# Kernel optimization log

Hardware: AMD Instinct MI355X
Metric: run time of the kernel (lower is better)

Reference implementation:

```python
import jax, jax.numpy as jnp
import numpy as np

N = 65536          # particles
E = 524288         # relations (avg degree 8)
RIG = 4096         # rigid instance = particles [0, RIG); fluid = [RIG, N)
PSTEPS = 2
ATTR, STATE, RELD, NF = 3, 6, 1, 128
DT = 1.0 / 60.0
MEAN_P = np.zeros(3, np.float32); STD_P = np.ones(3, np.float32)
MEAN_V = np.zeros(3, np.float32); STD_V = np.ones(3, np.float32)


def _lin(x, w, b):
    return x @ w.T + b  # torch Linear convention: w is [out, in]


def setup_inputs() -> dict:
    key = jax.random.key(0)
    ks = iter(jax.random.split(key, 40))
    d = {}
    d["state"] = jax.random.normal(next(ks), (N, STATE), jnp.float32)
    d["attr"] = jax.random.normal(next(ks), (N, ATTR), jnp.float32)
    d["Ra"] = jax.random.normal(next(ks), (E, RELD), jnp.float32)
    d["rel_recv"] = jax.random.randint(next(ks), (E,), 0, N, jnp.int32)
    d["rel_send"] = jax.random.randint(next(ks), (E,), 0, N, jnp.int32)

    def w(shape):
        return jax.random.normal(next(ks), shape, jnp.float32) / np.sqrt(shape[1])

    d["pe_w0"] = w((NF, ATTR + 2 * STATE)); d["pe_b0"] = jnp.zeros(NF)
    d["pe_w1"] = w((NF, NF)); d["pe_b1"] = jnp.zeros(NF)
    d["re_w0"] = w((NF, 2 * ATTR + 4 * STATE + RELD)); d["re_b0"] = jnp.zeros(NF)
    d["re_w1"] = w((NF, NF)); d["re_b1"] = jnp.zeros(NF)
    d["re_w2"] = w((NF, NF)); d["re_b2"] = jnp.zeros(NF)
    d["rp_w"] = w((NF, 3 * NF)); d["rp_b"] = jnp.zeros(NF)
    d["pp_w"] = w((NF, 2 * NF)); d["pp_b"] = jnp.zeros(NF)
    d["rg_w0"] = w((NF, NF)); d["rg_b0"] = jnp.zeros(NF)
    d["rg_w1"] = w((NF, NF)); d["rg_b1"] = jnp.zeros(NF)
    d["rg_w2"] = w((7, NF)); d["rg_b2"] = jnp.zeros(7)
    d["fl_w0"] = w((NF, NF)); d["fl_b0"] = jnp.zeros(NF)
    d["fl_w1"] = w((NF, NF)); d["fl_b1"] = jnp.zeros(NF)
    d["fl_w2"] = w((3, NF)); d["fl_b2"] = jnp.zeros(3)
    return d


def reference(state, attr, Ra, rel_recv, rel_send,
              pe_w0, pe_b0, pe_w1, pe_b1,
              re_w0, re_b0, re_w1, re_b1, re_w2, re_b2,
              rp_w, rp_b, pp_w, pp_b,
              rg_w0, rg_b0, rg_w1, rg_b1, rg_w2, rg_b2,
              fl_w0, fl_b0, fl_w1, fl_b1, fl_w2, fl_b2):
    relu = jax.nn.relu
    mean_p = jnp.asarray(MEAN_P); std_p = jnp.asarray(STD_P)
    mean_v = jnp.asarray(MEAN_V); std_v = jnp.asarray(STD_V)

    # rigid-body offset (state minus instance centroid for the rigid instance)
    offset = jnp.zeros_like(state).at[:RIG].set(
        state[:RIG] - jnp.mean(state[:RIG], axis=0))
    attr2 = jnp.concatenate([attr, offset], axis=1)        # [N, ATTR+STATE]

    # f_O^enc: particle encoder on [attr2, state]
    pe_in = jnp.concatenate([attr2, state], axis=1)         # [N, 15]
    particle_encode = relu(_lin(relu(_lin(pe_in, pe_w0, pe_b0)), pe_w1, pe_b1))

    # f_R^enc: relation encoder on gathered receiver/sender features
    rel_in = jnp.concatenate([attr2[rel_recv], attr2[rel_send],
                              state[rel_recv], state[rel_send], Ra], axis=1)  # [E, 31]
    h = relu(_lin(rel_in, re_w0, re_b0))
    h = relu(_lin(h, re_w1, re_b1))
    relation_encode = relu(_lin(h, re_w2, re_b2))           # [E, NF]

    # propagation: gather effects -> f_R -> scatter-add -> f_O
    effect = jnp.zeros((N, NF), state.dtype)
    for _ in range(PSTEPS):
        r_eff = effect[rel_recv]                            # [E, NF]
        s_eff = effect[rel_send]                            # [E, NF]
        rel_eff = relu(_lin(jnp.concatenate(
            [relation_encode, r_eff, s_eff], axis=1), rp_w, rp_b))
        agg = jax.ops.segment_sum(rel_eff, rel_recv, num_segments=N)  # Rr @ rel_eff
        effect = relu(_lin(jnp.concatenate(
            [particle_encode, agg], axis=1), pp_w, pp_b))   # residual=False

    # rigid predictor: quaternion + translation of the rigid body
    pooled = jnp.mean(effect[:RIG], axis=0)                 # [NF]
    t = _lin(relu(_lin(relu(_lin(pooled, rg_w0, rg_b0)), rg_w1, rg_b1)), rg_w2, rg_b2)
    q = t[:4] / jnp.linalg.norm(t[:4])
    w, x, y, z = q[0], q[1], q[2], q[3]
    R = jnp.stack([
        jnp.stack([1.0 - 2 * (y * y + z * z), 2 * (x * y + z * w), 2 * (x * z - y * w)]),
        jnp.stack([2 * (x * y - z * w), 1.0 - 2 * (x * x + z * z), 2 * (y * z + x * w)]),
        jnp.stack([2 * (x * z + y * w), 2 * (y * z - x * w), 1.0 - 2 * (x * x + y * y)]),
    ])
    b = t[4:] * std_p
    p0 = state[:RIG, :3] * std_p + mean_p
    c = jnp.mean(p0, axis=0)
    p1 = (p0 - c) @ R + b + c
    v = (p1 - p0) / DT
    pred_rigid = (v - mean_v) / std_v                       # [RIG, 3]

    # fluid predictor: per-particle MLP
    f = relu(_lin(effect[RIG:], fl_w0, fl_b0))
    f = relu(_lin(f, fl_w1, fl_b1))
    pred_fluid = _lin(f, fl_w2, fl_b2)                      # [N-RIG, 3]

    return jnp.concatenate([pred_rigid, pred_fluid], axis=0)  # [N, 3]
```

## Files before the change

kernel.cpp:

```cpp
#include <hip/hip_runtime.h>
#include <hip/hip_bf16.h>
#include <cstdio>

#define N_P   65536
#define N_E   524288
#define RIG_  4096

typedef __attribute__((ext_vector_type(8))) short bf16x8;
typedef __attribute__((ext_vector_type(4))) float f32x4;
typedef unsigned short u16;
typedef unsigned int   u32;

__device__ __forceinline__ u16 f2b(float x) {
    __hip_bfloat16 h = __float2bfloat16(x);
    return *(u16*)&h;
}
__device__ __forceinline__ float b2f(u16 u) {
    union { unsigned u; float f; } c; c.u = ((unsigned)u) << 16; return c.f;
}
__device__ __forceinline__ unsigned pk2(float x, float y) {
    return (unsigned)f2b(x) | ((unsigned)f2b(y) << 16);
}
#define MFMA(a,b,c) __builtin_amdgcn_mfma_f32_16x16x32_bf16((a),(b),(c),0,0,0)

__device__ __forceinline__ void bar_l() {
    asm volatile("s_waitcnt lgkmcnt(0)\n\ts_barrier" ::: "memory");
}

__global__ __launch_bounds__(256) void k_hist(const int* __restrict__ recv,
                                              u32* __restrict__ cnt) {
    int i = blockIdx.x * 256 + threadIdx.x;
    if (i < N_E) atomicAdd(&cnt[recv[i]], 1u);
}
__global__ __launch_bounds__(256) void k_scan1(u32* __restrict__ data,
                                               u32* __restrict__ bsum) {
    __shared__ u32 s[256];
    int t = threadIdx.x, g = blockIdx.x * 256 + t;
    u32 v = data[g];
    s[t] = v; __syncthreads();
    for (int o = 1; o < 256; o <<= 1) {
        u32 x = (t >= o) ? s[t - o] : 0u;
        __syncthreads(); s[t] += x; __syncthreads();
    }
    data[g] = s[t] - v;
    if (t == 255) bsum[blockIdx.x] = s[255];
}
__global__ __launch_bounds__(256) void k_scan2(u32* __restrict__ bsum) {
    __shared__ u32 s[256];
    int t = threadIdx.x;
    u32 v = bsum[t];
    s[t] = v; __syncthreads();
    for (int o = 1; o < 256; o <<= 1) {
        u32 x = (t >= o) ? s[t - o] : 0u;
        __syncthreads(); s[t] += x; __syncthreads();
    }
    bsum[t] = s[t] - v;
}
__global__ __launch_bounds__(256) void k_scan3(u32* __restrict__ data,
                                               const u32* __restrict__ bsum) {
    int g = blockIdx.x * 256 + threadIdx.x;
    data[g] += bsum[blockIdx.x];
}
__global__ __launch_bounds__(256) void k_scatter(const int* __restrict__ recv,
                                                 const int* __restrict__ send,
                                                 u32* __restrict__ head,
                                                 int4* __restrict__ edges) {
    int i = blockIdx.x * 256 + threadIdx.x;
    if (i < N_E) {
        int n = recv[i];
        u32 pos = atomicAdd(&head[n], 1u);
        edges[pos] = make_int4(n, send[i], i, 0);
    }
}

struct CvtJob { const float* src; u16* dst; int n; int mode; int bstart; };
struct CvtArgs { CvtJob j[14]; };

__global__ __launch_bounds__(256) void k_cvt_all(CvtArgs a) {
    int b = blockIdx.x;
    int ji = 0;
    #pragma unroll
    for (int k = 1; k < 14; k++) if (b >= a.j[k].bstart) ji = k;
    CvtJob jb = a.j[ji];
    int i = (b - jb.bstart) * 256 + threadIdx.x;
    if (i >= jb.n) return;
    if (jb.mode == 0) {
        jb.dst[i] = f2b(jb.src[i]);
    } else if (jb.mode == 2) {
        int r = i >> 7;
        jb.dst[i] = (r < 3) ? f2b(jb.src[i]) : 0;
    } else if (jb.mode == 3) {
        int r = i >> 7, c = i & 127;
        jb.dst[i] = f2b(jb.src[r * 384 + c]);
    } else if (jb.mode == 4) {
        int r = i >> 7, c = i & 127;
        jb.dst[i] = f2b(jb.src[r * 256 + c]);
    } else if (jb.mode == 5) {
        int r = i >> 5, c = i & 31;
        float v = 0.f;
        if (c < 9)       v = jb.src[r * 31 + c];
        else if (c < 15) v = jb.src[r * 31 + 18 + (c - 9)];
        jb.dst[i] = f2b(v);
    } else if (jb.mode == 6) {
        int r = i >> 5, c = i & 31;
        float v = 0.f;
        if (c < 9)       v = jb.src[r * 31 + 9 + c];
        else if (c < 15) v = jb.src[r * 31 + 24 + (c - 9)];
        jb.dst[i] = f2b(v);
    } else {
        int r = i >> 5, c = i & 31;
        jb.dst[i] = (c < 15) ? f2b(jb.src[r * 15 + c]) : 0;
    }
}

__global__ __launch_bounds__(256) void k_centroid(const float* __restrict__ state,
                                                  float* __restrict__ cent) {
    int d = blockIdx.x;
    __shared__ float red[256];
    float s = 0.f;
    for (int r = threadIdx.x; r < RIG_; r += 256) s += state[r * 6 + d];
    red[threadIdx.x] = s; __syncthreads();
    for (int o = 128; o > 0; o >>= 1) {
        if (threadIdx.x < o) red[threadIdx.x] += red[threadIdx.x + o];
        __syncthreads();
    }
    if (threadIdx.x == 0) cent[d] = red[0] / (float)RIG_;
}

__global__ __launch_bounds__(256) void k_particle_ext(
        const float* __restrict__ state, const float* __restrict__ attr,
        const float* __restrict__ cent,
        const u16* __restrict__ w0r, const u16* __restrict__ w0s,
        const u16* __restrict__ pew0, const float* __restrict__ pe_b0,
        const u16* __restrict__ pew1, const float* __restrict__ pe_b1,
        const u16* __restrict__ wp,
        u16* __restrict__ P, u16* __restrict__ Q, u16* __restrict__ T) {
    __shared__ float in_s[64][16];
    __shared__ u16 INF[64 * 32];
    __shared__ __align__(16) u16 BUF[64 * 128];
    __shared__ float b0_s[128], b1_s[128];
    int t = threadIdx.x;
    int base = blockIdx.x * 64;
    if (t < 128) { b0_s[t] = pe_b0[t]; b1_s[t] = pe_b1[t]; }
    for (int it = t; it < 64 * 15; it += 256) {
        int r = it / 15, c = it % 15;
        int p = base + r;
        float v;
        if (c < 3)      v = attr[p * 3 + c];
        else if (c < 9) v = (p < RIG_) ? (state[p * 6 + (c - 3)] - cent[c - 3]) : 0.0f;
        else            v = state[p * 6 + (c - 9)];
        in_s[r][c] = v;
    }
    __syncthreads();
    int wv = t >> 6, kq4 = (t >> 4) & 3, m = t & 15;
    {
        int e = wv * 16 + m;
        u16 tmp[8];
        #pragma unroll
        for (int j = 0; j < 8; j++) {
            int k = kq4 * 8 + j;
            tmp[j] = (k < 15) ? f2b(in_s[e][k]) : (u16)0;
        }
        *(uint4*)&INF[((wv * 4 + kq4) * 16 + m) * 8] = *(uint4*)tmp;
    }
    int lane = t & 63, mm = lane & 15, quad = lane >> 4;
    bf16x8 af0 = *(const bf16x8*)&INF[((wv * 4 + quad) * 16 + mm) * 8];
    {
        f32x4 acc[8] = {};
        #pragma unroll
        for (int nt = 0; nt < 8; nt++) {
            bf16x8 bf = *(const bf16x8*)(w0r + (size_t)(nt * 16 + mm) * 32 + quad * 8);
            acc[nt] = MFMA(af0, bf, acc[nt]);
        }
        #pragma unroll
        for (int nt = 0; nt < 8; nt++) {
            int col = nt * 16 + mm;
            #pragma unroll
            for (int rg = 0; rg < 4; rg++) {
                int row = wv * 16 + quad * 4 + rg;
                P[(size_t)(base + row) * 128 + col] = f2b(acc[nt][rg]);
            }
        }
    }
    {
        f32x4 acc[8] = {};
        #pragma unroll
        for (int nt = 0; nt < 8; nt++) {
            bf16x8 bf = *(const bf16x8*)(w0s + (size_t)(nt * 16 + mm) * 32 + quad * 8);
            acc[nt] = MFMA(af0, bf, acc[nt]);
        }
        #pragma unroll
        for (int nt = 0; nt < 8; nt++) {
            int col = nt * 16 + mm;
            #pragma unroll
            for (int rg = 0; rg < 4; rg++) {
                int row = wv * 16 + quad * 4 + rg;
                Q[(size_t)(base + row) * 128 + col] = f2b(acc[nt][rg]);
            }
        }
    }
    {
        f32x4 acc[8] = {};
        #pragma unroll
        for (int nt = 0; nt < 8; nt++) {
            bf16x8 bf = *(const bf16x8*)(pew0 + (size_t)(nt * 16 + mm) * 32 + quad * 8);
            acc[nt] = MFMA(af0, bf, acc[nt]);
        }
        #pragma unroll
        for (int nt = 0; nt < 8; nt++) {
            int col = nt * 16 + mm;
            #pragma unroll
            for (int rg = 0; rg < 4; rg++) {
                BUF[((wv * 16 + (col >> 3)) * 16 + quad * 4 + rg) * 8 + (col & 7)] =
                    f2b(fmaxf(acc[nt][rg] + b0_s[col], 0.f));
            }
        }
    }
    {
        f32x4 acc[8] = {};
        for (int kc = 0; kc < 4; kc++) {
            bf16x8 af = *(const bf16x8*)&BUF[((wv * 16 + kc * 4 + quad) * 16 + mm) * 8];
            #pragma unroll
            for (int nt = 0; nt < 8; nt++) {
                bf16x8 bf = *(const bf16x8*)(pew1 + (size_t)(nt * 16 + mm) * 128 + kc * 32 + quad * 8);
                acc[nt] = MFMA(af, bf, acc[nt]);
            }
        }
        #pragma unroll
        for (int nt = 0; nt < 8; nt++) {
            int col = nt * 16 + mm;
            #pragma unroll
            for (int rg = 0; rg < 4; rg++) {
                BUF[((wv * 16 + (col >> 3)) * 16 + quad * 4 + rg) * 8 + (col & 7)] =
                    f2b(fmaxf(acc[nt][rg] + b1_s[col], 0.f));
            }
        }
    }
    {
        f32x4 acc[8] = {};
        for (int kc = 0; kc < 4; kc++) {
            bf16x8 af = *(const bf16x8*)&BUF[((wv * 16 + kc * 4 + quad) * 16 + mm) * 8];
            #pragma unroll
            for (int nt = 0; nt < 8; nt++) {
                bf16x8 bf = *(const bf16x8*)(wp + (size_t)(nt * 16 + mm) * 128 + kc * 32 + quad * 8);
                acc[nt] = MFMA(af, bf, acc[nt]);
            }
        }
        #pragma unroll
        for (int nt = 0; nt < 8; nt++) {
            int col = nt * 16 + mm;
            #pragma unroll
            for (int rg = 0; rg < 4; rg++) {
                int row = wv * 16 + quad * 4 + rg;
                T[(size_t)(base + row) * 128 + col] = f2b(acc[nt][rg]);
            }
        }
    }
}

__global__ __launch_bounds__(512, 4) void k_rel(
        const u16* __restrict__ P, const u16* __restrict__ Q,
        const float* __restrict__ Ra, const int4* __restrict__ edges,
        const float* __restrict__ re_w0_raw, const float* __restrict__ b0,
        const u16* __restrict__ w1b, const float* __restrict__ b1,
        const u16* __restrict__ w2b, const float* __restrict__ b2,
        const u16* __restrict__ wreb, const float* __restrict__ rpb,
        u16* __restrict__ Z, float* __restrict__ agg) {
    __shared__ __align__(16) u16 BUFA[64 * 136];
    __shared__ __align__(16) u16 BUFB[64 * 136];
    __shared__ int rv_s[2][64];
    __shared__ float wRa_s[128], b0_s[128], rpb_s[128];
    int t = threadIdx.x;
    if (t < 128) {
        wRa_s[t] = re_w0_raw[t * 31 + 30];
        b0_s[t] = b0[t]; rpb_s[t] = rpb[t];
    }
    int w = t >> 6, lane = t & 63, mm = lane & 15, quad = lane >> 4;
    int colw = w * 16 + mm;
    bf16x8 W1f[4], W2f[4], WEf[4];
    #pragma unroll
    for (int kc = 0; kc < 4; kc++) {
        W1f[kc] = *(const bf16x8*)(w1b  + (size_t)colw * 128 + kc * 32 + quad * 8);
        W2f[kc] = *(const bf16x8*)(w2b  + (size_t)colw * 128 + kc * 32 + quad * 8);
        WEf[kc] = *(const bf16x8*)(wreb + (size_t)colw * 128 + kc * 32 + quad * 8);
    }
    float b1c = b1[colw], b2c = b2[colw];
    int es = t >> 3, cs2 = (t & 7) * 2;
    int egs = es >> 4, ms = es & 15;
    int sseg = t >> 7, cseg = t & 127;
    int zrow = t >> 3, zc0 = (t & 7) * 16;
    const long NT = N_E / 64;
    const long stride = gridDim.x;

    long tile = blockIdx.x;
    uint4 upC0, upC1, uqC0, uqC1; float raC; int rvC;
    {
        long nb = tile * 64;
        int4 e = edges[nb + es];
        rvC = edges[nb + (t & 63)].x;
        raC = Ra[e.z];
        upC0 = *(const uint4*)(P + (size_t)e.x * 128 + (size_t)cs2 * 8);
        upC1 = *(const uint4*)(P + (size_t)e.x * 128 + (size_t)(cs2 + 1) * 8);
        uqC0 = *(const uint4*)(Q + (size_t)e.y * 128 + (size_t)cs2 * 8);
        uqC1 = *(const uint4*)(Q + (size_t)e.y * 128 + (size_t)(cs2 + 1) * 8);
    }
    __syncthreads();
    int p = 0;
    for (; tile < NT; tile += stride) {
        long base = tile * 64;
        long ntile = tile + stride;
        bool hn = ntile < NT;
        int4 eN = make_int4(0, 0, 0, 0); int rvN = 0;
        if (hn) {
            long nb = ntile * 64;
            eN  = edges[nb + es];
            rvN = edges[nb + (t & 63)].x;
        }
        if (t < 64) rv_s[p][t] = rvC;
        {
            #pragma unroll
            for (int ci = 0; ci < 2; ci++) {
                int kq = cs2 + ci;
                uint4 up = ci ? upC1 : upC0;
                uint4 uq = ci ? uqC1 : uqC0;
                const u16* pp = (const u16*)&up; const u16* qq = (const u16*)&uq;
                u16 outv[8];
                #pragma unroll
                for (int j = 0; j < 8; j++) {
                    int c = kq * 8 + j;
                    float v = b2f(pp[j]) + b2f(qq[j]) + raC * wRa_s[c] + b0_s[c];
                    outv[j] = f2b(fmaxf(v, 0.f));
                }
                *(uint4*)&BUFA[((egs * 16 + kq) * 16 + ms) * 8] = *(uint4*)outv;
            }
        }
        bar_l();
        uint4 upN0{}, upN1{}, uqN0{}, uqN1{}; float raN = 0.f;
        if (hn) {
            raN  = Ra[eN.z];
            upN0 = *(const uint4*)(P + (size_t)eN.x * 128 + (size_t)cs2 * 8);
            upN1 = *(const uint4*)(P + (size_t)eN.x * 128 + (size_t)(cs2 + 1) * 8);
            uqN0 = *(const uint4*)(Q + (size_t)eN.y * 128 + (size_t)cs2 * 8);
            uqN1 = *(const uint4*)(Q + (size_t)eN.y * 128 + (size_t)(cs2 + 1) * 8);
        }
        {
            f32x4 acc[4] = {};
            #pragma unroll
            for (int eg = 0; eg < 4; eg++)
                #pragma unroll
                for (int kc = 0; kc < 4; kc++) {
                    bf16x8 af = *(const bf16x8*)&BUFA[((eg * 16 + kc * 4 + quad) * 16 + mm) * 8];
                    acc[eg] = MFMA(af, W1f[kc], acc[eg]);
                }
            #pragma unroll
            for (int eg = 0; eg < 4; eg++)
                #pragma unroll
                for (int rg = 0; rg < 4; rg++)
                    BUFB[((eg * 16 + (colw >> 3)) * 16 + quad * 4 + rg) * 8 + (colw & 7)] =
                        f2b(fmaxf(acc[eg][rg] + b1c, 0.f));
        }
        bar_l();
        {
            f32x4 acc[4] = {};
            #pragma unroll
            for (int eg = 0; eg < 4; eg++)
                #pragma unroll
                for (int kc = 0; kc < 4; kc++) {
                    bf16x8 af = *(const bf16x8*)&BUFB[((eg * 16 + kc * 4 + quad) * 16 + mm) * 8];
                    acc[eg] = MFMA(af, W2f[kc], acc[eg]);
                }
            #pragma unroll
            for (int eg = 0; eg < 4; eg++)
                #pragma unroll
                for (int rg = 0; rg < 4; rg++)
                    BUFA[((eg * 16 + (colw >> 3)) * 16 + quad * 4 + rg) * 8 + (colw & 7)] =
                        f2b(fmaxf(acc[eg][rg] + b2c, 0.f));
        }
        bar_l();
        {
            f32x4 zacc[4] = {};
            #pragma unroll
            for (int eg = 0; eg < 4; eg++)
                #pragma unroll
                for (int kc = 0; kc < 4; kc++) {
                    bf16x8 af = *(const bf16x8*)&BUFA[((eg * 16 + kc * 4 + quad) * 16 + mm) * 8];
                    zacc[eg] = MFMA(af, WEf[kc], zacc[eg]);
                }
            #pragma unroll
            for (int eg = 0; eg < 4; eg++)
                #pragma unroll
                for (int rg = 0; rg < 4; rg++)
                    BUFB[(eg * 16 + quad * 4 + rg) * 136 + colw] = f2b(zacc[eg][rg]);
        }
        bar_l();
        {
            uint4 z0 = *(const uint4*)&BUFB[zrow * 136 + zc0];
            uint4 z1 = *(const uint4*)&BUFB[zrow * 136 + zc0 + 8];
            *(uint4*)&Z[(base + zrow) * 128 + zc0]     = z0;
            *(uint4*)&Z[(base + zrow) * 128 + zc0 + 8] = z1;
        }
        {
            int r0 = sseg * 16;
            int cur = rv_s[p][r0];
            float a = fmaxf(b2f(BUFB[r0 * 136 + cseg]) + rpb_s[cseg], 0.f);
            bool first = true;
            for (int rr = r0 + 1; rr < r0 + 16; rr++) {
                int n = rv_s[p][rr];
                float v = fmaxf(b2f(BUFB[rr * 136 + cseg]) + rpb_s[cseg], 0.f);
                if (n == cur) a += v;
                else {
                    if (first) atomicAdd(&agg[(size_t)cur * 128 + cseg], a);
                    else       agg[(size_t)cur * 128 + cseg] = a;
                    first = false; cur = n; a = v;
                }
            }
            atomicAdd(&agg[(size_t)cur * 128 + cseg], a);
        }
        if (hn) { upC0 = upN0; upC1 = upN1; uqC0 = uqN0; uqC1 = uqN1; raC = raN; rvC = rvN; }
        p ^= 1;
    }
}

__global__ __launch_bounds__(512, 4) void k_node2(
        const float* __restrict__ agg, const u16* __restrict__ T,
        const u16* __restrict__ wab, const float* __restrict__ ppb,
        const u16* __restrict__ wrb, const u16* __restrict__ wsb,
        u16* __restrict__ U, u16* __restrict__ V) {
    __shared__ __align__(16) u16 BUFA[64 * 128];
    __shared__ __align__(16) u16 BUFB[64 * 128];
    int t = threadIdx.x;
    int w = t >> 6, lane = t & 63, mm = lane & 15, quad = lane >> 4;
    int colw = w * 16 + mm;
    bf16x8 WAf[4], WRf[4], WSf[4];
    #pragma unroll
    for (int kc = 0; kc < 4; kc++) {
        WAf[kc] = *(const bf16x8*)(wab + (size_t)colw * 128 + kc * 32 + quad * 8);
        WRf[kc] = *(const bf16x8*)(wrb + (size_t)colw * 128 + kc * 32 + quad * 8);
        WSf[kc] = *(const bf16x8*)(wsb + (size_t)colw * 128 + kc * 32 + quad * 8);
    }
    float ppbc = ppb[colw];
    int es = t >> 3, cs2 = (t & 7) * 2;
    int egs = es >> 4, ms = es & 15;
    const int NTL = N_P / 64;
    for (int tile = blockIdx.x; tile < NTL; tile += gridDim.x) {
        long base = (long)tile * 64;
        __syncthreads();
        #pragma unroll
        for (int ci = 0; ci < 2; ci++) {
            int kq = cs2 + ci;
            const float* src = agg + (base + es) * 128 + kq * 8;
            float4 f0 = *(const float4*)src, f1 = *(const float4*)(src + 4);
            uint4 v;
            v.x = pk2(f0.x, f0.y); v.y = pk2(f0.z, f0.w);
            v.z = pk2(f1.x, f1.y); v.w = pk2(f1.z, f1.w);
            *(uint4*)&BUFA[((egs * 16 + kq) * 16 + ms) * 8] = v;
        }
        bar_l();
        {
            f32x4 acc[4] = {};
            #pragma unroll
            for (int eg = 0; eg < 4; eg++)
                #pragma unroll
                for (int kc = 0; kc < 4; kc++) {
                    bf16x8 af = *(const bf16x8*)&BUFA[((eg * 16 + kc * 4 + quad) * 16 + mm) * 8];
                    acc[eg] = MFMA(af, WAf[kc], acc[eg]);
                }
            #pragma unroll
            for (int eg = 0; eg < 4; eg++)
                #pragma unroll
                for (int rg = 0; rg < 4; rg++) {
                    long row = base + eg * 16 + quad * 4 + rg;
                    float v = acc[eg][rg] + b2f(T[row * 128 + colw]) + ppbc;
                    BUFB[((eg * 16 + (colw >> 3)) * 16 + quad * 4 + rg) * 8 + (colw & 7)] =
                        f2b(fmaxf(v, 0.f));
                }
        }
        bar_l();
        {
            f32x4 au[4] = {}, av[4] = {};
            #pragma unroll
            for (int eg = 0; eg < 4; eg++)
                #pragma unroll
                for (int kc = 0; kc < 4; kc++) {
                    bf16x8 af = *(const bf16x8*)&BUFB[((eg * 16 + kc * 4 + quad) * 16 + mm) * 8];
                    au[eg] = MFMA(af, WRf[kc], au[eg]);
                    av[eg] = MFMA(af, WSf[kc], av[eg]);
                }
            #pragma unroll
            for (int eg = 0; eg < 4; eg++)
                #pragma unroll
                for (int rg = 0; rg < 4; rg++) {
                    long row = base + eg * 16 + quad * 4 + rg;
                    U[row * 128 + colw] = f2b(au[eg][rg]);
                    V[row * 128 + colw] = f2b(av[eg][rg]);
                }
        }
    }
}

#define HPAD 136
__global__ __launch_bounds__(256) void k_node2fl(
        const float* __restrict__ agg, const u16* __restrict__ T,
        const u16* __restrict__ wab, const float* __restrict__ ppb,
        float* __restrict__ pooledsum,
        const u16* __restrict__ w0b, const float* __restrict__ b0,
        const u16* __restrict__ w1b, const float* __restrict__ b1,
        const u16* __restrict__ w2b, const float* __restrict__ b2,
        float* __restrict__ out) {
    __shared__ __align__(16) u16 H[64 * HPAD];
    int t = threadIdx.x;
    long base = (long)blockIdx.x * 64;
    bool fluid = (base >= RIG_);
    int wv = t >> 6, kq4 = (t >> 4) & 3, m = t & 15;
    {
        long node = base + wv * 16 + m;
        #pragma unroll
        for (int i = 0; i < 4; i++) {
            int kq = kq4 + 4 * i;
            const float* src = agg + node * 128 + kq * 8;
            float4 f0 = *(const float4*)src, f1 = *(const float4*)(src + 4);
            uint4 v;
            v.x = pk2(f0.x, f0.y); v.y = pk2(f0.z, f0.w);
            v.z = pk2(f1.x, f1.y); v.w = pk2(f1.z, f1.w);
            *(uint4*)&H[((wv * 16 + kq) * 16 + m) * 8] = v;
        }
    }
    int lane = t & 63, mm = lane & 15, quad = lane >> 4;
    f32x4 acc[8] = {};
    for (int kc = 0; kc < 4; kc++) {
        bf16x8 af = *(const bf16x8*)&H[((wv * 16 + kc * 4 + quad) * 16 + mm) * 8];
        #pragma unroll
        for (int nt = 0; nt < 8; nt++) {
            bf16x8 bf = *(const bf16x8*)(wab + (size_t)(nt * 16 + mm) * 128 + kc * 32 + quad * 8);
            acc[nt] = MFMA(af, bf, acc[nt]);
        }
    }
    __syncthreads();
    #pragma unroll
    for (int nt = 0; nt < 8; nt++) {
        int col = nt * 16 + mm;
        #pragma unroll
        for (int rg = 0; rg < 4; rg++) {
            long row = base + wv * 16 + quad * 4 + rg;
            float v = acc[nt][rg] + b2f(T[row * 128 + col]) + ppb[col];
            H[(wv * 16 + quad * 4 + rg) * HPAD + col] = f2b(fmaxf(v, 0.f));
        }
    }
    if (!fluid) {
        bar_l();
        int col = t & 127, half = t >> 7;
        float s = 0.f;
        for (int r = half * 32; r < half * 32 + 32; r++)
            s += b2f(H[r * HPAD + col]);
        atomicAdd(&pooledsum[col], s);
        return;
    }
    {
        f32x4 a8[8] = {};
        for (int kc = 0; kc < 4; kc++) {
            bf16x8 af = *(const bf16x8*)&H[(wv * 16 + mm) * HPAD + kc * 32 + quad * 8];
            #pragma unroll
            for (int nt = 0; nt < 8; nt++) {
                bf16x8 bf = *(const bf16x8*)(w0b + (size_t)(nt * 16 + mm) * 128 + kc * 32 + quad * 8);
                a8[nt] = MFMA(af, bf, a8[nt]);
            }
        }
        #pragma unroll
        for (int nt = 0; nt < 8; nt++) {
            int col = nt * 16 + mm;
            float bv = b0[col];
            #pragma unroll
            for (int rg = 0; rg < 4; rg++) {
                int row = wv * 16 + quad * 4 + rg;
                H[row * HPAD + col] = f2b(fmaxf(a8[nt][rg] + bv, 0.f));
            }
        }
    }
    {
        f32x4 a8[8] = {};
        for (int kc = 0; kc < 4; kc++) {
            bf16x8 af = *(const bf16x8*)&H[(wv * 16 + mm) * HPAD + kc * 32 + quad * 8];
            #pragma unroll
            for (int nt = 0; nt < 8; nt++) {
                bf16x8 bf = *(const bf16x8*)(w1b + (size_t)(nt * 16 + mm) * 128 + kc * 32 + quad * 8);
                a8[nt] = MFMA(af, bf, a8[nt]);
            }
        }
        #pragma unroll
        for (int nt = 0; nt < 8; nt++) {
            int col = nt * 16 + mm;
            float bv = b1[col];
            #pragma unroll
            for (int rg = 0; rg < 4; rg++) {
                int row = wv * 16 + quad * 4 + rg;
                H[row * HPAD + col] = f2b(fmaxf(a8[nt][rg] + bv, 0.f));
            }
        }
    }
    {
        f32x4 a1 = {};
        for (int kc = 0; kc < 4; kc++) {
            bf16x8 af = *(const bf16x8*)&H[(wv * 16 + mm) * HPAD + kc * 32 + quad * 8];
            bf16x8 bf = *(const bf16x8*)(w2b + (size_t)mm * 128 + kc * 32 + quad * 8);
            a1 = MFMA(af, bf, a1);
        }
        if (mm < 3) {
            float bv = b2[mm];
            #pragma unroll
            for (int rg = 0; rg < 4; rg++) {
                long row = base + wv * 16 + quad * 4 + rg;
                out[row * 3 + mm] = a1[rg] + bv;
            }
        }
    }
}

__global__ __launch_bounds__(256) void k_edge2(
        const u16* __restrict__ Z, const u16* __restrict__ U, const u16* __restrict__ V,
        const int4* __restrict__ edges,
        const float* __restrict__ rpb, float* __restrict__ agg) {
    __shared__ __align__(16) u16 S16[64 * 136];
    __shared__ int rv_s[64];
    __shared__ float rpb_s[128];
    int t = threadIdx.x;
    long base = (long)blockIdx.x * 64;
    if (t < 64) rv_s[t] = edges[base + t].x;
    if (t < 128) rpb_s[t] = rpb[t];
    int r = t >> 2, q = t & 3;
    int4 er = edges[base + r];
    long zb = (base + r) * 128;
    size_t ub = (size_t)er.x * 128, vb = (size_t)er.y * 128;
    bar_l();
    #pragma unroll
    for (int i = 0; i < 4; i++) {
        int c0 = q * 32 + i * 8;
        uint4 uz = *(const uint4*)(Z + zb + c0);
        uint4 uu = *(const uint4*)(U + ub + c0);
        uint4 uv = *(const uint4*)(V + vb + c0);
        const u16* zz = (const u16*)&uz; const u16* pu = (const u16*)&uu; const u16* pv = (const u16*)&uv;
        u16 o[8];
        #pragma unroll
        for (int j = 0; j < 8; j++)
            o[j] = f2b(fmaxf(b2f(zz[j]) + b2f(pu[j]) + b2f(pv[j]) + rpb_s[c0 + j], 0.f));
        *(uint4*)&S16[r * 136 + c0] = *(uint4*)o;
    }
    bar_l();
    {
        int s = t >> 7, col = t & 127;
        int r0 = s * 32;
        int cur = rv_s[r0];
        float a = b2f(S16[r0 * 136 + col]);
        bool first = true;
        for (int rr = r0 + 1; rr < r0 + 32; rr++) {
            int n = rv_s[rr];
            float v = b2f(S16[rr * 136 + col]);
            if (n == cur) a += v;
            else {
                if (first) atomicAdd(&agg[(size_t)cur * 128 + col], a);
                else       agg[(size_t)cur * 128 + col] = a;
                first = false; cur = n; a = v;
            }
        }
        atomicAdd(&agg[(size_t)cur * 128 + col], a);
    }
}

__global__ __launch_bounds__(128) void k_rigid_head(
        const float* __restrict__ pooledsum,
        const float* __restrict__ w0, const float* __restrict__ b0,
        const float* __restrict__ w1, const float* __restrict__ b1,
        const float* __restrict__ w2, const float* __restrict__ b2,
        float* __restrict__ rig) {
    __shared__ float pl[128], ha[128], hb[128], tv[7];
    int t = threadIdx.x;
    pl[t] = pooledsum[t] * (1.0f / (float)RIG_);
    __syncthreads();
    float a = b0[t];
    for (int k = 0; k < 128; k++) a += w0[t * 128 + k] * pl[k];
    ha[t] = fmaxf(a, 0.f);
    __syncthreads();
    a = b1[t];
    for (int k = 0; k < 128; k++) a += w1[t * 128 + k] * ha[k];
    hb[t] = fmaxf(a, 0.f);
    __syncthreads();
    if (t < 7) {
        float s = b2[t];
        for (int k = 0; k < 128; k++) s += w2[t * 128 + k] * hb[k];
        tv[t] = s;
    }
    __syncthreads();
    if (t == 0) {
        float w = tv[0], x = tv[1], y = tv[2], z = tv[3];
        float n = sqrtf(w * w + x * x + y * y + z * z);
        w /= n; x /= n; y /= n; z /= n;
        rig[0] = 1.f - 2.f * (y * y + z * z); rig[1] = 2.f * (x * y + z * w); rig[2] = 2.f * (x * z - y * w);
        rig[3] = 2.f * (x * y - z * w); rig[4] = 1.f - 2.f * (x * x + z * z); rig[5] = 2.f * (y * z + x * w);
        rig[6] = 2.f * (x * z + y * w); rig[7] = 2.f * (y * z - x * w); rig[8] = 1.f - 2.f * (x * x + y * y);
        rig[9] = tv[4]; rig[10] = tv[5]; rig[11] = tv[6];
    }
}

__global__ __launch_bounds__(256) void k_rigid_out(
        const float* __restrict__ state, const float* __restrict__ cent,
        const float* __restrict__ rig, float* __restrict__ out) {
    int i = blockIdx.x * 256 + threadIdx.x;
    if (i >= RIG_) return;
    float p0[3], d[3];
    #pragma unroll
    for (int k = 0; k < 3; k++) { p0[k] = state[i * 6 + k]; d[k] = p0[k] - cent[k]; }
    #pragma unroll
    for (int j = 0; j < 3; j++) {
        float p1 = rig[0 * 3 + j] * d[0] + rig[1 * 3 + j] * d[1] + rig[2 * 3 + j] * d[2]
                 + rig[9 + j] + cent[j];
        out[i * 3 + j] = (p1 - p0[j]) * 60.0f;
    }
}

extern "C" void kernel_launch(void* const* d_in, const int* in_sizes, int n_in,
                              void* d_out, int out_size, void* d_ws, size_t ws_size,
                              hipStream_t stream) {
    const float* state = (const float*)d_in[0];
    const float* attr  = (const float*)d_in[1];
    const float* Ra    = (const float*)d_in[2];
    const int*   recv  = (const int*)d_in[3];
    const int*   send  = (const int*)d_in[4];
    const float* pe_w0 = (const float*)d_in[5];  const float* pe_b0 = (const float*)d_in[6];
    const float* pe_w1 = (const float*)d_in[7];  const float* pe_b1 = (const float*)d_in[8];
    const float* re_w0 = (const float*)d_in[9];  const float* re_b0 = (const float*)d_in[10];
    const float* re_w1 = (const float*)d_in[11]; const float* re_b1 = (const float*)d_in[12];
    const float* re_w2 = (const float*)d_in[13]; const float* re_b2 = (const float*)d_in[14];
    const float* rp_w  = (const float*)d_in[15]; const float* rp_b  = (const float*)d_in[16];
    const float* pp_w  = (const float*)d_in[17]; const float* pp_b  = (const float*)d_in[18];
    const float* rg_w0 = (const float*)d_in[19]; const float* rg_b0 = (const float*)d_in[20];
    const float* rg_w1 = (const float*)d_in[21]; const float* rg_b1 = (const float*)d_in[22];
    const float* rg_w2 = (const float*)d_in[23]; const float* rg_b2 = (const float*)d_in[24];
    const float* fl_w0 = (const float*)d_in[25]; const float* fl_b0 = (const float*)d_in[26];
    const float* fl_w1 = (const float*)d_in[27]; const float* fl_b1 = (const float*)d_in[28];
    const float* fl_w2 = (const float*)d_in[29]; const float* fl_b2 = (const float*)d_in[30];
    float* out = (float*)d_out;

    char* p = (char*)d_ws;
    auto alloc = [&](size_t bytes) { char* r = p; p += (bytes + 255) / 256 * 256; return r; };
    float* cent    = (float*)alloc(8 * 4);
    float* pooled  = (float*)alloc(128 * 4);
    float* rig     = (float*)alloc(16 * 4);
    u32*   rowhead = (u32*)alloc((size_t)N_P * 4);
    u32*   bsum    = (u32*)alloc(256 * 4);
    int4*  edges   = (int4*)alloc((size_t)N_E * 16);
    float* agg     = (float*)alloc((size_t)N_P * 128 * 4);
    u16*   Z       = (u16*)alloc((size_t)N_E * 128 * 2);
    u16*   T       = (u16*)alloc((size_t)N_P * 128 * 2);
    u16*   P       = (u16*)alloc((size_t)N_P * 128 * 2);
    u16*   Q       = (u16*)alloc((size_t)N_P * 128 * 2);
    u16*   wreb    = (u16*)alloc(128 * 128 * 2);
    u16*   wrb     = (u16*)alloc(128 * 128 * 2);
    u16*   wsb     = (u16*)alloc(128 * 128 * 2);
    u16*   wpb     = (u16*)alloc(128 * 128 * 2);
    u16*   wab     = (u16*)alloc(128 * 128 * 2);
    u16*   rw1b    = (u16*)alloc(128 * 128 * 2);
    u16*   rw2b    = (u16*)alloc(128 * 128 * 2);
    u16*   pew1b   = (u16*)alloc(128 * 128 * 2);
    u16*   flw0b   = (u16*)alloc(128 * 128 * 2);
    u16*   flw1b   = (u16*)alloc(128 * 128 * 2);
    u16*   flw2b   = (u16*)alloc(16 * 128 * 2);
    u16*   w0rb    = (u16*)alloc(128 * 32 * 2);
    u16*   w0sb    = (u16*)alloc(128 * 32 * 2);
    u16*   pew0b   = (u16*)alloc(128 * 32 * 2);
    size_t need = (size_t)(p - (char*)d_ws);
    if (ws_size < need) {
        fprintf(stderr, "kernel_launch: ws_size %zu < needed %zu\n", ws_size, need);
        return;
    }
    u16* U = P; u16* V = Q;

    hipMemsetAsync(rowhead, 0, (size_t)N_P * 4, stream);
    k_hist<<<N_E / 256, 256, 0, stream>>>(recv, rowhead);
    k_scan1<<<N_P / 256, 256, 0, stream>>>(rowhead, bsum);
    k_scan2<<<1, 256, 0, stream>>>(bsum);
    k_scan3<<<N_P / 256, 256, 0, stream>>>(rowhead, bsum);
    k_scatter<<<N_E / 256, 256, 0, stream>>>(recv, send, rowhead, edges);

    CvtArgs ca;
    int bs = 0;
    auto addjob = [&](int idx, const float* s, u16* d, int n, int mode) {
        ca.j[idx] = {s, d, n, mode, bs};
        bs += (n + 255) / 256;
    };
    addjob(0,  rp_w,        wreb,  128 * 128, 3);
    addjob(1,  rp_w + 128,  wrb,   128 * 128, 3);
    addjob(2,  rp_w + 256,  wsb,   128 * 128, 3);
    addjob(3,  pp_w,        wpb,   128 * 128, 4);
    addjob(4,  pp_w + 128,  wab,   128 * 128, 4);
    addjob(5,  re_w1,       rw1b,  128 * 128, 0);
    addjob(6,  re_w2,       rw2b,  128 * 128, 0);
    addjob(7,  pe_w1,       pew1b, 128 * 128, 0);
    addjob(8,  fl_w0,       flw0b, 128 * 128, 0);
    addjob(9,  fl_w1,       flw1b, 128 * 128, 0);
    addjob(10, fl_w2,       flw2b, 16 * 128,  2);
    addjob(11, re_w0,       w0rb,  128 * 32,  5);
    addjob(12, re_w0,       w0sb,  128 * 32,  6);
    addjob(13, pe_w0,       pew0b, 128 * 32,  7);
    k_cvt_all<<<bs, 256, 0, stream>>>(ca);

    k_centroid<<<6, 256, 0, stream>>>(state, cent);
    k_particle_ext<<<N_P / 64, 256, 0, stream>>>(state, attr, cent,
                                                 w0rb, w0sb, pew0b, pe_b0,
                                                 pew1b, pe_b1, wpb, P, Q, T);

    hipMemsetAsync(agg, 0, (size_t)N_P * 128 * 4, stream);
    k_rel<<<512, 512, 0, stream>>>(P, Q, Ra, edges,
                                   re_w0, re_b0, rw1b, re_b1, rw2b, re_b2,
                                   wreb, rp_b, Z, agg);
    k_node2<<<512, 512, 0, stream>>>(agg, T, wab, pp_b, wrb, wsb, U, V);

    hipMemsetAsync(agg, 0, (size_t)N_P * 128 * 4, stream);
    hipMemsetAsync(pooled, 0, 128 * 4, stream);
    k_edge2<<<N_E / 64, 256, 0, stream>>>(Z, U, V, edges, rp_b, agg);
    k_node2fl<<<N_P / 64, 256, 0, stream>>>(agg, T, wab, pp_b, pooled,
                                            flw0b, fl_b0, flw1b, fl_b1,
                                            flw2b, fl_b2, out);

    k_rigid_head<<<1, 128, 0, stream>>>(pooled, rg_w0, rg_b0, rg_w1, rg_b1, rg_w2, rg_b2, rig);
    k_rigid_out<<<(RIG_ + 255) / 256, 256, 0, stream>>>(state, cent, rig, out);
}
```

Before: 513.0 us.

## Make particle encoder and fluid head persistent with register-resident weight fragments

Converts k_particle_ext and k_node2fl into persistent 512-thread kernels over a 512-block grid. Each wave owns a 16-column output slice and keeps its weight fragments in registers across tiles, instead of re-reading the full weight matrices from global memory for every 64-row tile. Each wave now computes all four 16-row groups of a tile for its column slice, using double LDS buffers and block barriers between layers. The rigid pooling reduction is redone with wave shuffles. This raises register pressure and adds extra barriers per tile.

```diff
diff --git a/kernel.cpp b/kernel.cpp
--- a/kernel.cpp
+++ b/kernel.cpp
@@ -127,7 +127,7 @@
     if (threadIdx.x == 0) cent[d] = red[0] / (float)RIG_;
 }
 
-__global__ __launch_bounds__(256) void k_particle_ext(
+__global__ __launch_bounds__(512, 4) void k_particle_ext(
         const float* __restrict__ state, const float* __restrict__ attr,
         const float* __restrict__ cent,
         const u16* __restrict__ w0r, const u16* __restrict__ w0s,
@@ -137,123 +137,114 @@
         u16* __restrict__ P, u16* __restrict__ Q, u16* __restrict__ T) {
     __shared__ float in_s[64][16];
     __shared__ u16 INF[64 * 32];
-    __shared__ __align__(16) u16 BUF[64 * 128];
-    __shared__ float b0_s[128], b1_s[128];
+    __shared__ __align__(16) u16 BUFA[64 * 128];
+    __shared__ __align__(16) u16 BUFB[64 * 128];
     int t = threadIdx.x;
-    int base = blockIdx.x * 64;
-    if (t < 128) { b0_s[t] = pe_b0[t]; b1_s[t] = pe_b1[t]; }
-    for (int it = t; it < 64 * 15; it += 256) {
-        int r = it / 15, c = it % 15;
-        int p = base + r;
-        float v;
-        if (c < 3)      v = attr[p * 3 + c];
-        else if (c < 9) v = (p < RIG_) ? (state[p * 6 + (c - 3)] - cent[c - 3]) : 0.0f;
-        else            v = state[p * 6 + (c - 9)];
-        in_s[r][c] = v;
-    }
-    __syncthreads();
-    int wv = t >> 6, kq4 = (t >> 4) & 3, m = t & 15;
-    {
-        int e = wv * 16 + m;
-        u16 tmp[8];
+    int w = t >> 6, lane = t & 63, mm = lane & 15, quad = lane >> 4;
+    int colw = w * 16 + mm;
+    bf16x8 W0Rf = *(const bf16x8*)(w0r  + (size_t)colw * 32 + quad * 8);
+    bf16x8 W0Sf = *(const bf16x8*)(w0s  + (size_t)colw * 32 + quad * 8);
+    bf16x8 PE0f = *(const bf16x8*)(pew0 + (size_t)colw * 32 + quad * 8);
+    bf16x8 PE1f[4], WPf[4];
+    #pragma unroll
+    for (int kc = 0; kc < 4; kc++) {
+        PE1f[kc] = *(const bf16x8*)(pew1 + (size_t)colw * 128 + kc * 32 + quad * 8);
+        WPf[kc]  = *(const bf16x8*)(wp   + (size_t)colw * 128 + kc * 32 + quad * 8);
+    }
+    float b0c = pe_b0[colw], b1c = pe_b1[colw];
+    const int NTL = N_P / 64;
+    for (int tile = blockIdx.x; tile < NTL; tile += gridDim.x) {
+        int base = tile * 64;
+        bar_l();
+        for (int it = t; it < 64 * 15; it += 512) {
+            int r = it / 15, c = it % 15;
+            int p = base + r;
+            float v;
+            if (c < 3)      v = attr[p * 3 + c];
+            else if (c < 9) v = (p < RIG_) ? (state[p * 6 + (c - 3)] - cent[c - 3]) : 0.0f;
+            else            v = state[p * 6 + (c - 9)];
+            in_s[r][c] = v;
+        }
+        bar_l();
+        if (t < 256) {
+            int wv = t >> 6, kq4 = (t >> 4) & 3, m = t & 15;
+            int e = wv * 16 + m;
+            u16 tmp[8];
+            #pragma unroll
+            for (int j = 0; j < 8; j++) {
+                int k = kq4 * 8 + j;
+                tmp[j] = (k < 15) ? f2b(in_s[e][k]) : (u16)0;
+            }
+            *(uint4*)&INF[((wv * 4 + kq4) * 16 + m) * 8] = *(uint4*)tmp;
+        }
+        bar_l();
+        bf16x8 af0[4];
         #pragma unroll
-        for (int j = 0; j < 8; j++) {
-            int k = kq4 * 8 + j;
-            tmp[j] = (k < 15) ? f2b(in_s[e][k]) : (u16)0;
-        }
-        *(uint4*)&INF[((wv * 4 + kq4) * 16 + m) * 8] = *(uint4*)tmp;
-    }
-    int lane = t & 63, mm = lane & 15, quad = lane >> 4;
-    bf16x8 af0 = *(const bf16x8*)&INF[((wv * 4 + quad) * 16 + mm) * 8];
-    {
-        f32x4 acc[8] = {};
-        #pragma unroll
-        for (int nt = 0; nt < 8; nt++) {
-            bf16x8 bf = *(const bf16x8*)(w0r + (size_t)(nt * 16 + mm) * 32 + quad * 8);
-            acc[nt] = MFMA(af0, bf, acc[nt]);
-        }
-        #pragma unroll
-        for (int nt = 0; nt < 8; nt++) {
-            int col = nt * 16 + mm;
-            #pragma unroll
-            for (int rg = 0; rg < 4; rg++) {
-                int row = wv * 16 + quad * 4 + rg;
-                P[(size_t)(base + row) * 128 + col] = f2b(acc[nt][rg]);
-            }
-        }
-    }
-    {
-        f32x4 acc[8] = {};
-        #pragma unroll
-        for (int nt = 0; nt < 8; nt++) {
-            bf16x8 bf = *(const bf16x8*)(w0s + (size_t)(nt * 16 + mm) * 32 + quad * 8);
-            acc[nt] = MFMA(af0, bf, acc[nt]);
-        }
-        #pragma unroll
-        for (int nt = 0; nt < 8; nt++) {
-            int col = nt * 16 + mm;
-            #pragma unroll
-            for (int rg = 0; rg < 4; rg++) {
-                int row = wv * 16 + quad * 4 + rg;
-                Q[(size_t)(base + row) * 128 + col] = f2b(acc[nt][rg]);
-            }
-        }
-    }
-    {
-        f32x4 acc[8] = {};
-        #pragma unroll
-        for (int nt = 0; nt < 8; nt++) {
-            bf16x8 bf = *(const bf16x8*)(pew0 + (size_t)(nt * 16 + mm) * 32 + quad * 8);
-            acc[nt] = MFMA(af0, bf, acc[nt]);
-        }
-        #pragma unroll
-        for (int nt = 0; nt < 8; nt++) {
-            int col = nt * 16 + mm;
-            #pragma unroll
-            for (int rg = 0; rg < 4; rg++) {
-                BUF[((wv * 16 + (col >> 3)) * 16 + quad * 4 + rg) * 8 + (col & 7)] =
-                    f2b(fmaxf(acc[nt][rg] + b0_s[col], 0.f));
-            }
-        }
-    }
-    {
-        f32x4 acc[8] = {};
-        for (int kc = 0; kc < 4; kc++) {
-            bf16x8 af = *(const bf16x8*)&BUF[((wv * 16 + kc * 4 + quad) * 16 + mm) * 8];
-            #pragma unroll
-            for (int nt = 0; nt < 8; nt++) {
-                bf16x8 bf = *(const bf16x8*)(pew1 + (size_t)(nt * 16 + mm) * 128 + kc * 32 + quad * 8);
-                acc[nt] = MFMA(af, bf, acc[nt]);
-            }
-        }
-        #pragma unroll
-        for (int nt = 0; nt < 8; nt++) {
-            int col = nt * 16 + mm;
-            #pragma unroll
-            for (int rg = 0; rg < 4; rg++) {
-                BUF[((wv * 16 + (col >> 3)) * 16 + quad * 4 + rg) * 8 + (col & 7)] =
-                    f2b(fmaxf(acc[nt][rg] + b1_s[col], 0.f));
-            }
-        }
-    }
-    {
-        f32x4 acc[8] = {};
-        for (int kc = 0; kc < 4; kc++) {
-            bf16x8 af = *(const bf16x8*)&BUF[((wv * 16 + kc * 4 + quad) * 16 + mm) * 8];
-            #pragma unroll
-            for (int nt = 0; nt < 8; nt++) {
-                bf16x8 bf = *(const bf16x8*)(wp + (size_t)(nt * 16 + mm) * 128 + kc * 32 + quad * 8);
-                acc[nt] = MFMA(af, bf, acc[nt]);
-            }
-        }
-        #pragma unroll
-        for (int nt = 0; nt < 8; nt++) {
-            int col = nt * 16 + mm;
-            #pragma unroll
-            for (int rg = 0; rg < 4; rg++) {
-                int row = wv * 16 + quad * 4 + rg;
-                T[(size_t)(base + row) * 128 + col] = f2b(acc[nt][rg]);
-            }
+        for (int eg = 0; eg < 4; eg++)
+            af0[eg] = *(const bf16x8*)&INF[((eg * 4 + quad) * 16 + mm) * 8];
+        {
+            f32x4 a[4] = {};
+            #pragma unroll
+            for (int eg = 0; eg < 4; eg++) a[eg] = MFMA(af0[eg], W0Rf, a[eg]);
+            #pragma unroll
+            for (int eg = 0; eg < 4; eg++)
+                #pragma unroll
+                for (int rg = 0; rg < 4; rg++)
+                    P[(size_t)(base + eg * 16 + quad * 4 + rg) * 128 + colw] = f2b(a[eg][rg]);
+        }
+        {
+            f32x4 a[4] = {};
+            #pragma unroll
+            for (int eg = 0; eg < 4; eg++) a[eg] = MFMA(af0[eg], W0Sf, a[eg]);
+            #pragma unroll
+            for (int eg = 0; eg < 4; eg++)
+                #pragma unroll
+                for (int rg = 0; rg < 4; rg++)
+                    Q[(size_t)(base + eg * 16 + quad * 4 + rg) * 128 + colw] = f2b(a[eg][rg]);
+        }
+        {
+            f32x4 a[4] = {};
+            #pragma unroll
+            for (int eg = 0; eg < 4; eg++) a[eg] = MFMA(af0[eg], PE0f, a[eg]);
+            #pragma unroll
+            for (int eg = 0; eg < 4; eg++)
+                #pragma unroll
+                for (int rg = 0; rg < 4; rg++)
+                    BUFA[((eg * 16 + (colw >> 3)) * 16 + quad * 4 + rg) * 8 + (colw & 7)] =
+                        f2b(fmaxf(a[eg][rg] + b0c, 0.f));
+        }
+        bar_l();
+        {
+            f32x4 a[4] = {};
+            #pragma unroll
+            for (int eg = 0; eg < 4; eg++)
+                #pragma unroll
+                for (int kc = 0; kc < 4; kc++) {
+                    bf16x8 af = *(const bf16x8*)&BUFA[((eg * 16 + kc * 4 + quad) * 16 + mm) * 8];
+                    a[eg] = MFMA(af, PE1f[kc], a[eg]);
+                }
+            #pragma unroll
+            for (int eg = 0; eg < 4; eg++)
+                #pragma unroll
+                for (int rg = 0; rg < 4; rg++)
+                    BUFB[((eg * 16 + (colw >> 3)) * 16 + quad * 4 + rg) * 8 + (colw & 7)] =
+                        f2b(fmaxf(a[eg][rg] + b1c, 0.f));
+        }
+        bar_l();
+        {
+            f32x4 a[4] = {};
+            #pragma unroll
+            for (int eg = 0; eg < 4; eg++)
+                #pragma unroll
+                for (int kc = 0; kc < 4; kc++) {
+                    bf16x8 af = *(const bf16x8*)&BUFB[((eg * 16 + kc * 4 + quad) * 16 + mm) * 8];
+                    a[eg] = MFMA(af, WPf[kc], a[eg]);
+                }
+            #pragma unroll
+            for (int eg = 0; eg < 4; eg++)
+                #pragma unroll
+                for (int rg = 0; rg < 4; rg++)
+                    T[(size_t)(base + eg * 16 + quad * 4 + rg) * 128 + colw] = f2b(a[eg][rg]);
         }
     }
 }
@@ -498,8 +489,7 @@
     }
 }
 
-#define HPAD 136
-__global__ __launch_bounds__(256) void k_node2fl(
+__global__ __launch_bounds__(512, 4) void k_node2fl(
         const float* __restrict__ agg, const u16* __restrict__ T,
         const u16* __restrict__ wab, const float* __restrict__ ppb,
         float* __restrict__ pooledsum,
@@ -507,109 +497,119 @@
         const u16* __restrict__ w1b, const float* __restrict__ b1,
         const u16* __restrict__ w2b, const float* __restrict__ b2,
         float* __restrict__ out) {
-    __shared__ __align__(16) u16 H[64 * HPAD];
+    __shared__ __align__(16) u16 BUFA[64 * 128];
+    __shared__ __align__(16) u16 BUFB[64 * 128];
     int t = threadIdx.x;
-    long base = (long)blockIdx.x * 64;
-    bool fluid = (base >= RIG_);
-    int wv = t >> 6, kq4 = (t >> 4) & 3, m = t & 15;
-    {
-        long node = base + wv * 16 + m;
+    int w = t >> 6, lane = t & 63, mm = lane & 15, quad = lane >> 4;
+    int colw = w * 16 + mm;
+    bf16x8 WAf[4], W0f[4], W1f[4];
+    #pragma unroll
+    for (int kc = 0; kc < 4; kc++) {
+        WAf[kc] = *(const bf16x8*)(wab + (size_t)colw * 128 + kc * 32 + quad * 8);
+        W0f[kc] = *(const bf16x8*)(w0b + (size_t)colw * 128 + kc * 32 + quad * 8);
+        W1f[kc] = *(const bf16x8*)(w1b + (size_t)colw * 128 + kc * 32 + quad * 8);
+    }
+    float ppbc = ppb[colw], b0c = b0[colw], b1c = b1[colw];
+    int es = t >> 3, cs2 = (t & 7) * 2;
+    int egs = es >> 4, ms = es & 15;
+    const int NTL = N_P / 64;
+    for (int tile = blockIdx.x; tile < NTL; tile += gridDim.x) {
+        long base = (long)tile * 64;
+        bool fluid = base >= RIG_;
+        bar_l();
         #pragma unroll
-        for (int i = 0; i < 4; i++) {
-            int kq = kq4 + 4 * i;
-            const float* src = agg + node * 128 + kq * 8;
+        for (int ci = 0; ci < 2; ci++) {
+            int kq = cs2 + ci;
+            const float* src = agg + (base + es) * 128 + kq * 8;
             float4 f0 = *(const float4*)src, f1 = *(const float4*)(src + 4);
             uint4 v;
             v.x = pk2(f0.x, f0.y); v.y = pk2(f0.z, f0.w);
             v.z = pk2(f1.x, f1.y); v.w = pk2(f1.z, f1.w);
-            *(uint4*)&H[((wv * 16 + kq) * 16 + m) * 8] = v;
-        }
-    }
-    int lane = t & 63, mm = lane & 15, quad = lane >> 4;
-    f32x4 acc[8] = {};
-    for (int kc = 0; kc < 4; kc++) {
-        bf16x8 af = *(const bf16x8*)&H[((wv * 16 + kc * 4 + quad) * 16 + mm) * 8];
+            *(uint4*)&BUFA[((egs * 16 + kq) * 16 + ms) * 8] = v;
+        }
+        bar_l();
+        f32x4 acc[4] = {};
         #pragma unroll
-        for (int nt = 0; nt < 8; nt++) {
-            bf16x8 bf = *(const bf16x8*)(wab + (size_t)(nt * 16 + mm) * 128 + kc * 32 + quad * 8);
-            acc[nt] = MFMA(af, bf, acc[nt]);
-        }
-    }
-    __syncthreads();
-    #pragma unroll
-    for (int nt = 0; nt < 8; nt++) {
-        int col = nt * 16 + mm;
+        for (int eg = 0; eg < 4; eg++)
+            #pragma unroll
+            for (int kc = 0; kc < 4; kc++) {
+                bf16x8 af = *(const bf16x8*)&BUFA[((eg * 16 + kc * 4 + quad) * 16 + mm) * 8];
+                acc[eg] = MFMA(af, WAf[kc], acc[eg]);
+            }
+        if (!fluid) {
+            float s = 0.f;
+            #pragma unroll
+            for (int eg = 0; eg < 4; eg++)
+                #pragma unroll
+                for (int rg = 0; rg < 4; rg++) {
+                    long row = base + eg * 16 + quad * 4 + rg;
+                    float v = acc[eg][rg] + b2f(T[row * 128 + colw]) + ppbc;
+                    s += b2f(f2b(fmaxf(v, 0.f)));
+                }
+            s += __shfl_xor(s, 16);
+            s += __shfl_xor(s, 32);
+            if (quad == 0) atomicAdd(&pooledsum[colw], s);
+            continue;
+        }
         #pragma unroll
-        for (int rg = 0; rg < 4; rg++) {
-            long row = base + wv * 16 + quad * 4 + rg;
-            float v = acc[nt][rg] + b2f(T[row * 128 + col]) + ppb[col];
-            H[(wv * 16 + quad * 4 + rg) * HPAD + col] = f2b(fmaxf(v, 0.f));
-        }
-    }
-    if (!fluid) {
-        bar_l();
-        int col = t & 127, half = t >> 7;
-        float s = 0.f;
-        for (int r = half * 32; r < half * 32 + 32; r++)
-            s += b2f(H[r * HPAD + col]);
-        atomicAdd(&pooledsum[col], s);
-        return;
-    }
-    {
-        f32x4 a8[8] = {};
-        for (int kc = 0; kc < 4; kc++) {
-            bf16x8 af = *(const bf16x8*)&H[(wv * 16 + mm) * HPAD + kc * 32 + quad * 8];
-            #pragma unroll
-            for (int nt = 0; nt < 8; nt++) {
-                bf16x8 bf = *(const bf16x8*)(w0b + (size_t)(nt * 16 + mm) * 128 + kc * 32 + quad * 8);
-                a8[nt] = MFMA(af, bf, a8[nt]);
+        for (int eg = 0; eg < 4; eg++)
+            #pragma unroll
+            for (int rg = 0; rg < 4; rg++) {
+                long row = base + eg * 16 + quad * 4 + rg;
+                float v = acc[eg][rg] + b2f(T[row * 128 + colw]) + ppbc;
+                BUFB[((eg * 16 + (colw >> 3)) * 16 + quad * 4 + rg) * 8 + (colw & 7)] =
+                    f2b(fmaxf(v, 0.f));
             }
-        }
-        #pragma unroll
-        for (int nt = 0; nt < 8; nt++) {
-            int col = nt * 16 + mm;
-            float bv = b0[col];
-            #pragma unroll
-            for (int rg = 0; rg < 4; rg++) {
-                int row = wv * 16 + quad * 4 + rg;
-                H[row * HPAD + col] = f2b(fmaxf(a8[nt][rg] + bv, 0.f));
+        bar_l();
+        {
+            f32x4 a[4] = {};
+            #pragma unroll
+            for (int eg = 0; eg < 4; eg++)
+                #pragma unroll
+                for (int kc = 0; kc < 4; kc++) {
+                    bf16x8 af = *(const bf16x8*)&BUFB[((eg * 16 + kc * 4 + quad) * 16 + mm) * 8];
+                    a[eg] = MFMA(af, W0f[kc], a[eg]);
+                }
+            #pragma unroll
+            for (int eg = 0; eg < 4; eg++)
+                #pragma unroll
+                for (int rg = 0; rg < 4; rg++)
+                    BUFA[((eg * 16 + (colw >> 3)) * 16 + quad * 4 + rg) * 8 + (colw & 7)] =
+                        f2b(fmaxf(a[eg][rg] + b0c, 0.f));
+        }
+        bar_l();
+        {
+            f32x4 a[4] = {};
+            #pragma unroll
+            for (int eg = 0; eg < 4; eg++)
+                #pragma unroll
+                for (int kc = 0; kc < 4; kc++) {
+                    bf16x8 af = *(const bf16x8*)&BUFA[((eg * 16 + kc * 4 + quad) * 16 + mm) * 8];
+                    a[eg] = MFMA(af, W1f[kc], a[eg]);
+                }
+            #pragma unroll
+            for (int eg = 0; eg < 4; eg++)
+                #pragma unroll
+                for (int rg = 0; rg < 4; rg++)
+                    BUFB[((eg * 16 + (colw >> 3)) * 16 + quad * 4 + rg) * 8 + (colw & 7)] =
+                        f2b(fmaxf(a[eg][rg] + b1c, 0.f));
+        }
+        bar_l();
+        if (w < 4) {
+            f32x4 a1 = {};
+            #pragma unroll
+            for (int kc = 0; kc < 4; kc++) {
+                bf16x8 af = *(const bf16x8*)&BUFB[((w * 16 + kc * 4 + quad) * 16 + mm) * 8];
+                bf16x8 bf = *(const bf16x8*)(w2b + (size_t)mm * 128 + kc * 32 + quad * 8);
+                a1 = MFMA(af, bf, a1);
             }
-        }
-    }
-    {
-        f32x4 a8[8] = {};
-        for (int kc = 0; kc < 4; kc++) {
-            bf16x8 af = *(const bf16x8*)&H[(wv * 16 + mm) * HPAD + kc * 32 + quad * 8];
-            #pragma unroll
-            for (int nt = 0; nt < 8; nt++) {
-                bf16x8 bf = *(const bf16x8*)(w1b + (size_t)(nt * 16 + mm) * 128 + kc * 32 + quad * 8);
-                a8[nt] = MFMA(af, bf, a8[nt]);
-            }
-        }
-        #pragma unroll
-        for (int nt = 0; nt < 8; nt++) {
-            int col = nt * 16 + mm;
-            float bv = b1[col];
-            #pragma unroll
-            for (int rg = 0; rg < 4; rg++) {
-                int row = wv * 16 + quad * 4 + rg;
-                H[row * HPAD + col] = f2b(fmaxf(a8[nt][rg] + bv, 0.f));
-            }
-        }
-    }
-    {
-        f32x4 a1 = {};
-        for (int kc = 0; kc < 4; kc++) {
-            bf16x8 af = *(const bf16x8*)&H[(wv * 16 + mm) * HPAD + kc * 32 + quad * 8];
-            bf16x8 bf = *(const bf16x8*)(w2b + (size_t)mm * 128 + kc * 32 + quad * 8);
-            a1 = MFMA(af, bf, a1);
-        }
-        if (mm < 3) {
-            float bv = b2[mm];
-            #pragma unroll
-            for (int rg = 0; rg < 4; rg++) {
-                long row = base + wv * 16 + quad * 4 + rg;
-                out[row * 3 + mm] = a1[rg] + bv;
+            if (mm < 3) {
+                float bv = b2[mm];
+                #pragma unroll
+                for (int rg = 0; rg < 4; rg++) {
+                    long row = base + w * 16 + quad * 4 + rg;
+                    out[row * 3 + mm] = a1[rg] + bv;
+                }
             }
         }
     }
@@ -803,9 +803,9 @@
     k_cvt_all<<<bs, 256, 0, stream>>>(ca);
 
     k_centroid<<<6, 256, 0, stream>>>(state, cent);
-    k_particle_ext<<<N_P / 64, 256, 0, stream>>>(state, attr, cent,
-                                                 w0rb, w0sb, pew0b, pe_b0,
-                                                 pew1b, pe_b1, wpb, P, Q, T);
+    k_particle_ext<<<512, 512, 0, stream>>>(state, attr, cent,
+                                            w0rb, w0sb, pew0b, pe_b0,
+                                            pew1b, pe_b1, wpb, P, Q, T);
 
     hipMemsetAsync(agg, 0, (size_t)N_P * 128 * 4, stream);
     k_rel<<<512, 512, 0, stream>>>(P, Q, Ra, edges,
@@ -816,9 +816,9 @@
     hipMemsetAsync(agg, 0, (size_t)N_P * 128 * 4, stream);
     hipMemsetAsync(pooled, 0, 128 * 4, stream);
     k_edge2<<<N_E / 64, 256, 0, stream>>>(Z, U, V, edges, rp_b, agg);
-    k_node2fl<<<N_P / 64, 256, 0, stream>>>(agg, T, wab, pp_b, pooled,
-                                            flw0b, fl_b0, flw1b, fl_b1,
-                                            flw2b, fl_b2, out);
+    k_node2fl<<<512, 512, 0, stream>>>(agg, T, wab, pp_b, pooled,
+                                       flw0b, fl_b0, flw1b, fl_b1,
+                                       flw2b, fl_b2, out);
 
     k_rigid_head<<<1, 128, 0, stream>>>(pooled, rg_w0, rg_b0, rg_w1, rg_b1, rg_w2, rg_b2, rig);
     k_rigid_out<<<(RIG_ + 255) / 256, 256, 0, stream>>>(state, cent, rig, out);
```

New measurement: 467.6 us. 8.9% less time.
